# Optimization experiments

Measured on AMD Instinct MI355X. Metric: run time of the kernel, lower is better.

The kernel has to match this reference:

```python
import math
import jax, jax.numpy as jnp
import numpy as np

EPS = 1e-5  # BatchNorm2d default eps


def setup_inputs() -> dict:
    key = jax.random.key(0)
    ks = jax.random.split(key, 12)
    C, I = 256, 128  # in_channels, inter_channels (= C // reduction)
    n, h, w = 4, 64, 64
    s = 0.02
    return {
        "x": jax.random.normal(ks[0], (n, C, h, w), jnp.float32),
        "g_w": jax.random.normal(ks[1], (I, C), jnp.float32) * s,
        "g_b": jax.random.normal(ks[2], (I,), jnp.float32) * s,
        "theta_w": jax.random.normal(ks[3], (I, C), jnp.float32) * s,
        "theta_b": jax.random.normal(ks[4], (I,), jnp.float32) * s,
        "phi_w": jax.random.normal(ks[5], (I, C), jnp.float32) * s,
        "phi_b": jax.random.normal(ks[6], (I,), jnp.float32) * s,
        "out_w": jax.random.normal(ks[7], (C, I), jnp.float32) * s,
        "bn_gamma": jax.random.uniform(ks[8], (C,), jnp.float32, 0.5, 1.5),
        "bn_beta": jax.random.normal(ks[9], (C,), jnp.float32) * s,
        "bn_mean": jax.random.normal(ks[10], (C,), jnp.float32) * s,
        "bn_var": jax.random.uniform(ks[11], (C,), jnp.float32, 0.5, 1.5),
    }


def reference(x, g_w, g_b, theta_w, theta_b, phi_w, phi_b, out_w,
              bn_gamma, bn_beta, bn_mean, bn_var):
    n, c, h, w = x.shape
    xf = x.reshape(n, c, h * w)  # (n, C, N)

    def proj(Wm, b):  # 1x1 conv == per-position linear: (n, I, N)
        return jnp.einsum('ic,ncp->nip', Wm, xf) + b[None, :, None]

    g_x = proj(g_w, g_b)          # (n, I, N)
    theta_x = proj(theta_w, theta_b)  # (n, I, N)
    phi_x = proj(phi_w, phi_b)        # (n, I, N)

    # dot_product mode: softmax FIRST, then divide by sqrt(C) (faithful to source)
    scores = jnp.einsum('nip,niq->npq', theta_x, phi_x)  # (n, N, N)
    attn = jax.nn.softmax(scores, axis=-1) / math.sqrt(c)

    y = jnp.einsum('npq,niq->nip', attn, g_x)  # (n, I, N)
    y = y.reshape(n, -1, h, w)                 # (n, I, h, w)

    # conv_out: 1x1 conv (no bias) + BatchNorm2d (eval-mode running stats)
    y = jnp.einsum('oi,nihw->nohw', out_w, y)  # (n, C, h, w)
    inv = bn_gamma / jnp.sqrt(bn_var + EPS)
    y = y * inv[None, :, None, None] + (bn_beta - bn_mean * inv)[None, :, None, None]
    return y + x
```

## Files before the change

### kernel.cpp

```cpp
#include <hip/hip_runtime.h>

typedef short short8 __attribute__((ext_vector_type(8)));
typedef short short4v __attribute__((ext_vector_type(4)));
typedef float f32x4 __attribute__((ext_vector_type(4)));
typedef float f32x16 __attribute__((ext_vector_type(16)));
typedef unsigned int uint4v __attribute__((ext_vector_type(4)));
typedef unsigned int uint2v __attribute__((ext_vector_type(2)));

#define NB 4
#define CD 256
#define ID 128
#define NP 4096

static __device__ __forceinline__ short f2bf(float f){
  unsigned u = __float_as_uint(f);
  u += 0x7FFF + ((u >> 16) & 1);
  return (short)(u >> 16);
}
static __device__ __forceinline__ float bf2f(short s){
  unsigned u = ((unsigned)(unsigned short)s) << 16;
  return __uint_as_float(u);
}
static __device__ __forceinline__ unsigned cvtpk(float lo, float hi){
  unsigned r;
  asm("v_cvt_pk_bf16_f32 %0, %1, %2" : "=v"(r) : "v"(lo), "v"(hi));
  return r;
}
static __device__ __forceinline__ float fexp2(float x){
  float r;
  asm("v_exp_f32 %0, %1" : "=v"(r) : "v"(x));
  return r;
}
static __device__ __forceinline__ unsigned pack4_fp8(float a, float b, float c, float d){
  unsigned lo, hi;
  asm("v_cvt_pk_fp8_f32 %0, %1, %2" : "=v"(lo) : "v"(a), "v"(b));
  asm("v_cvt_pk_fp8_f32 %0, %1, %2" : "=v"(hi) : "v"(c), "v"(d));
  return (lo & 0xffffu) | (hi << 16);
}
static __device__ __forceinline__ unsigned char f2fp8(float v){
  unsigned u;
  asm("v_cvt_pk_fp8_f32 %0, %1, %1" : "=v"(u) : "v"(v));
  return (unsigned char)u;
}

static __device__ __forceinline__ void gload16(const void* g, void* l){
  __builtin_amdgcn_global_load_lds(
      (const __attribute__((address_space(1))) unsigned int*)g,
      (__attribute__((address_space(3))) unsigned int*)l, 16, 0, 0);
}

__global__ __launch_bounds__(256) void k_cvtw(const float* __restrict__ g_w,
    const float* __restrict__ th_w, const float* __restrict__ ph_w,
    const float* __restrict__ out_w, short* __restrict__ wb){
  int idx = (blockIdx.x * 256 + threadIdx.x) * 4;
  const float* s;
  int sel = idx >> 15;
  if(sel == 0) s = g_w; else if(sel == 1) s = th_w; else if(sel == 2) s = ph_w; else s = out_w;
  int off = idx & 32767;
  float4 v = *reinterpret_cast<const float4*>(s + off);
  short4v o = { f2bf(v.x), f2bf(v.y), f2bf(v.z), f2bf(v.w) };
  *reinterpret_cast<short4v*>(wb + idx) = o;
}

__global__ __launch_bounds__(256) void k_transpose(const float* __restrict__ x,
                                                   short* __restrict__ xt){
  __shared__ float T[64][68];
  int n = blockIdx.z, c0 = blockIdx.y * 64, p0 = blockIdx.x * 64;
  int t = threadIdx.x;
  const float* xp = x + ((size_t)(n * CD + c0)) * NP + p0;
#pragma unroll
  for(int it = 0; it < 4; ++it){
    int c = (t >> 4) + it * 16;
    int p = (t & 15) * 4;
    float4 v = *reinterpret_cast<const float4*>(xp + (size_t)c * NP + p);
    T[c][p+0] = v.x; T[c][p+1] = v.y; T[c][p+2] = v.z; T[c][p+3] = v.w;
  }
  __syncthreads();
  short* op = xt + ((size_t)(n * NP + p0)) * CD + c0;
  int p = t >> 2, cc = (t & 3) * 16;
  short8 a, b;
#pragma unroll
  for(int j = 0; j < 8; ++j){ a[j] = f2bf(T[cc + j][p]); b[j] = f2bf(T[cc + 8 + j][p]); }
  *reinterpret_cast<short8*>(op + (size_t)p * CD + cc) = a;
  *reinterpret_cast<short8*>(op + (size_t)p * CD + cc + 8) = b;
}

__global__ __launch_bounds__(512) void k_proj(const short* __restrict__ xt,
    const short* __restrict__ wb, const float* __restrict__ g_b,
    const float* __restrict__ th_b, const float* __restrict__ ph_b,
    unsigned char* __restrict__ q8, unsigned char* __restrict__ k8,
    unsigned char* __restrict__ v8){
  __shared__ __align__(16) char XT[32768];
  int b = blockIdx.x;
  int n = b >> 6, pt = b & 63;
  int pb0 = pt * 64;
  int t = threadIdx.x, w = t >> 6, l = t & 63;
  int lr = l & 15, lg = l >> 4;
  int i0 = w * 16;

  const char* xg = (const char*)(xt + ((size_t)(n * NP + pb0)) * CD);
#pragma unroll
  for(int i_ = 0; i_ < 4; ++i_){
    int dd = t * 16 + i_ * 8192;
    int row = dd >> 9;
    int sz = (dd & ~511) | ((dd & 511) ^ ((row & 15) << 4));
    gload16(xg + sz, XT + dd);
  }

  const short* gww = wb;
  const short* thw = wb + 32768;
  const short* phw = wb + 65536;
  short8 Wt[8], Wp[8], Wg[8];
#pragma unroll
  for(int kk = 0; kk < 8; ++kk){
    size_t wo = (size_t)(i0 + lr) * CD + kk * 32 + lg * 8;
    Wt[kk] = *reinterpret_cast<const short8*>(thw + wo);
    Wp[kk] = *reinterpret_cast<const short8*>(phw + wo);
    Wg[kk] = *reinterpret_cast<const short8*>(gww + wo);
  }
  float bt = th_b[i0 + lr] * 1.44269504f;
  float bp = ph_b[i0 + lr];
  float gb[4];
#pragma unroll
  for(int r = 0; r < 4; ++r) gb[r] = g_b[i0 + lg * 4 + r];

  __syncthreads();

  size_t pan = ((size_t)n * 64 + pt) * 64;
#pragma unroll
  for(int psub = 0; psub < 4; ++psub){
    int prow = psub * 16 + lr;
    short8 X[8];
#pragma unroll
    for(int kk = 0; kk < 8; ++kk)
      X[kk] = *reinterpret_cast<const short8*>(
          XT + prow * 512 + ((kk * 64 + lg * 16) ^ ((prow & 15) << 4)));
    f32x4 aT = {0.f,0.f,0.f,0.f}, aP = {0.f,0.f,0.f,0.f}, aG = {0.f,0.f,0.f,0.f};
#pragma unroll
    for(int kk = 0; kk < 8; ++kk){
      aT = __builtin_amdgcn_mfma_f32_16x16x32_bf16(X[kk], Wt[kk], aT, 0, 0, 0);
      aP = __builtin_amdgcn_mfma_f32_16x16x32_bf16(X[kk], Wp[kk], aP, 0, 0, 0);
      aG = __builtin_amdgcn_mfma_f32_16x16x32_bf16(Wg[kk], X[kk], aG, 0, 0, 0);
    }
#pragma unroll
    for(int r = 0; r < 4; ++r){
      size_t o = ((size_t)(n * NP + pb0 + psub * 16 + lg * 4 + r)) * ID + i0 + lr;
      q8[o] = f2fp8((aT[r] + bt * 0.69314718f * 1.44269504f));
    }
#pragma unroll
    for(int r = 0; r < 4; ++r){
      size_t o = ((size_t)(n * NP + pb0 + psub * 16 + lg * 4 + r)) * ID + i0 + lr;
      q8[o] = f2fp8((aT[r] + ph_b[0] * 0.f + th_b[i0 + lr]) * 1.44269504f);
      k8[o] = f2fp8(aP[r] + bp);
    }
#pragma unroll
    for(int r = 0; r < 4; ++r){
      int ii = i0 + lg * 4 + r;
      v8[(pan + (ii >> 1)) * 128 + (ii & 1) * 64 + psub * 16 + lr] = f2fp8(aG[r] + gb[r]);
    }
  }
}

__global__ __launch_bounds__(256, 2) void k_attn(const unsigned char* __restrict__ q8,
    const unsigned char* __restrict__ k8, const unsigned char* __restrict__ v8,
    short* __restrict__ po, float* __restrict__ psums){
  __shared__ __align__(16) char smem[65536];
  int b = blockIdx.x;
  int xcd = b & 7;
  int n = xcd >> 1;
  int kq = ((xcd & 1) << 1) | ((b >> 3) & 1);
  int qtl = b >> 4;
  int t = threadIdx.x, w = t >> 6, l = t & 63;
  int q31 = l & 31, hi = l >> 5;
  int pbase = qtl * 128 + w * 32;

  const char* kpanel = (const char*)k8 + ((size_t)(n * NP + kq * 1024)) * ID;
  const char* vpanel = (const char*)v8 + ((size_t)n * 64 + kq * 16) * 8192;
  const char* qbase  = (const char*)q8 + ((size_t)(n * NP + pbase)) * ID;

  uint2v Qf[8];
#pragma unroll
  for(int cst = 0; cst < 8; ++cst)
    Qf[cst] = *reinterpret_cast<const uint2v*>(qbase + q31 * 128 + cst * 16 + hi * 8);

  f32x16 Of[4];
#pragma unroll
  for(int db = 0; db < 4; ++db)
#pragma unroll
    for(int r = 0; r < 16; ++r) Of[db][r] = 0.f;
  float ps = 0.f;

#define STAGE(cb, kt_) do { \
    const char* kg_ = kpanel + (size_t)(kt_) * 8192; \
    const char* vg_ = vpanel + (size_t)(kt_) * 8192; \
    char* kld_ = smem + (cb) * 8192; \
    char* vld_ = smem + 16384 + (cb) * 8192; \
    _Pragma("unroll") \
    for(int i_ = 0; i_ < 2; ++i_){ \
      int dd = t * 16 + i_ * 4096; \
      int sz = (dd & ~127) | ((dd & 127) ^ (((dd >> 7) & 7) << 4)); \
      gload16(kg_ + sz, kld_ + dd); \
      gload16(vg_ + sz, vld_ + dd); \
    } \
  } while(0)

  STAGE(0, 0);
  __syncthreads();

#pragma unroll 2
  for(int kt = 0; kt < 16; ++kt){
    const int pb = kt & 1;
    if(kt + 1 < 16) STAGE(pb ^ 1, kt + 1);
    const char* Kc = smem + pb * 8192;
    const char* Vc = smem + 16384 + pb * 8192;
#pragma unroll
    for(int kb = 0; kb < 2; ++kb){
      f32x16 S;
#pragma unroll
      for(int r = 0; r < 16; ++r) S[r] = 0.f;
      int krow = kb * 32 + q31;
      __builtin_amdgcn_s_setprio(1);
#pragma unroll
      for(int cst = 0; cst < 8; ++cst){
        uint2v Kf = *reinterpret_cast<const uint2v*>(
            Kc + krow * 128 + ((cst * 16) ^ ((krow & 7) << 4)) + hi * 8);
        S = __builtin_amdgcn_mfma_f32_32x32x16_fp8_fp8(
            __builtin_bit_cast(long, Kf), __builtin_bit_cast(long, Qf[cst]), S, 0, 0, 0);
      }
      __builtin_amdgcn_s_setprio(0);
      float e[16];
#pragma unroll
      for(int r = 0; r < 16; ++r) e[r] = fexp2(S[r] - 4.0f);
#pragma unroll
      for(int r = 0; r < 16; ++r) ps += e[r];
      unsigned u0 = pack4_fp8(e[0],  e[1],  e[2],  e[3]);
      unsigned u1 = pack4_fp8(e[4],  e[5],  e[6],  e[7]);
      unsigned u2 = pack4_fp8(e[8],  e[9],  e[10], e[11]);
      unsigned u3 = pack4_fp8(e[12], e[13], e[14], e[15]);
      asm("v_permlane32_swap_b32 %0, %1" : "+v"(u0), "+v"(u1));
      asm("v_permlane32_swap_b32 %0, %1" : "+v"(u2), "+v"(u3));
      __builtin_amdgcn_s_setprio(1);
#pragma unroll
      for(int cc = 0; cc < 2; ++cc){
        uint2v Pa = cc ? uint2v{u2, u3} : uint2v{u0, u1};
        long Pl = __builtin_bit_cast(long, Pa);
#pragma unroll
        for(int db = 0; db < 4; ++db){
          int d = db * 32 + q31;
          int row = d >> 1;
          int off = (d & 1) * 64 + kb * 32 + cc * 16;
          uint2v Vf = *reinterpret_cast<const uint2v*>(
              Vc + row * 128 + ((off ^ ((row & 7) << 4))) + hi * 8);
          Of[db] = __builtin_amdgcn_mfma_f32_32x32x16_fp8_fp8(
              Pl, __builtin_bit_cast(long, Vf), Of[db], 0, 0, 0);
        }
      }
      __builtin_amdgcn_s_setprio(0);
    }
    __syncthreads();
  }
#undef STAGE

  float pst = ps + __shfl_xor(ps, 32);
  if(hi == 0)
    psums[(size_t)kq * 16384 + n * NP + pbase + q31] = pst;

  float* ow = (float*)(smem + w * 16384);
#pragma unroll
  for(int reg = 0; reg < 16; ++reg){
    int q = (reg & 3) + 8 * (reg >> 2) + 4 * hi;
#pragma unroll
    for(int db = 0; db < 4; ++db)
      ow[q * 128 + db * 32 + q31] = Of[db][reg];
  }
  asm volatile("s_waitcnt lgkmcnt(0)" ::: "memory");
  __builtin_amdgcn_sched_barrier(0);
  short* pr = po + ((size_t)kq * 16384 + n * NP + pbase) * ID;
#pragma unroll
  for(int it = 0; it < 8; ++it){
    int o = it * 1024 + l * 16;
    int q = o >> 8, d0 = (o & 255) >> 1;
    f32x4 va = *reinterpret_cast<const f32x4*>(ow + q * 128 + d0);
    f32x4 vb = *reinterpret_cast<const f32x4*>(ow + q * 128 + d0 + 4);
    uint4v pk4 = { cvtpk(va[0], va[1]), cvtpk(va[2], va[3]),
                   cvtpk(vb[0], vb[1]), cvtpk(vb[2], vb[3]) };
    *reinterpret_cast<short8*>(pr + (size_t)q * ID + d0) = __builtin_bit_cast(short8, pk4);
  }
}

__global__ __launch_bounds__(512) void k_outproj(const short* __restrict__ po,
    const float* __restrict__ psums, const short* __restrict__ ow_b,
    const float* __restrict__ bng, const float* __restrict__ bnb,
    const float* __restrict__ bnm, const float* __restrict__ bnv,
    const float* __restrict__ x, float* __restrict__ out){
  __shared__ __align__(16) short XW[64 * 128];
  int b = blockIdx.x;
  int n = b >> 6, pt = b & 63;
  int pg0 = pt * 64;
  int t = threadIdx.x, w = t >> 6, l = t & 63;
  int lr = l & 15, lg = l >> 4;

  {
    int p = t >> 3, i0 = (t & 7) * 16;
    size_t qg = (size_t)n * NP + pg0 + p;
    float den = psums[qg] + psums[16384 + qg] + psums[32768 + qg] + psums[49152 + qg];
    float inv = 1.f / (16.f * den);
    const short* pp = po + qg * ID + i0;
    int key = (p & 15) << 4;
#pragma unroll
    for(int h = 0; h < 2; ++h){
      short8 b0 = *reinterpret_cast<const short8*>(pp + h * 8);
      short8 b1 = *reinterpret_cast<const short8*>(pp + (size_t)16384 * ID + h * 8);
      short8 b2 = *reinterpret_cast<const short8*>(pp + (size_t)32768 * ID + h * 8);
      short8 b3 = *reinterpret_cast<const short8*>(pp + (size_t)49152 * ID + h * 8);
      float f[8];
#pragma unroll
      for(int j = 0; j < 8; ++j)
        f[j] = (bf2f(b0[j]) + bf2f(b1[j]) + bf2f(b2[j]) + bf2f(b3[j])) * inv;
      uint4v pkv = { cvtpk(f[0], f[1]), cvtpk(f[2], f[3]),
                     cvtpk(f[4], f[5]), cvtpk(f[6], f[7]) };
      *reinterpret_cast<short8*>((char*)XW + p * 256 + ((i0 * 2 + h * 16) ^ key)) =
          __builtin_bit_cast(short8, pkv);
    }
  }
  __syncthreads();

  int c0 = w * 32;
  f32x4 acc[2][4];
#pragma unroll
  for(int mf = 0; mf < 2; ++mf)
#pragma unroll
    for(int nf = 0; nf < 4; ++nf) acc[mf][nf] = {0.f,0.f,0.f,0.f};
#pragma unroll
  for(int kk = 0; kk < 4; ++kk){
    short8 Af[2];
#pragma unroll
    for(int mf = 0; mf < 2; ++mf)
      Af[mf] = *reinterpret_cast<const short8*>(ow_b + (size_t)(c0 + mf * 16 + lr) * ID + kk * 32 + lg * 8);
#pragma unroll
    for(int nf = 0; nf < 4; ++nf){
      int prow = nf * 16 + lr;
      short8 Bf = *reinterpret_cast<const short8*>(
          (char*)XW + prow * 256 + ((kk * 64 + lg * 16) ^ ((prow & 15) << 4)));
#pragma unroll
      for(int mf = 0; mf < 2; ++mf)
        acc[mf][nf] = __builtin_amdgcn_mfma_f32_16x16x32_bf16(Af[mf], Bf, acc[mf][nf], 0, 0, 0);
    }
  }

#pragma unroll
  for(int mf = 0; mf < 2; ++mf){
    int cb = c0 + mf * 16 + lg * 4;
    float inv[4], sh[4];
#pragma unroll
    for(int r = 0; r < 4; ++r){
      float iv = bng[cb + r] * rsqrtf(bnv[cb + r] + 1e-5f);
      inv[r] = iv;
      sh[r] = bnb[cb + r] - bnm[cb + r] * iv;
    }
#pragma unroll
    for(int nf = 0; nf < 4; ++nf){
      int p = pg0 + nf * 16 + lr;
#pragma unroll
      for(int r = 0; r < 4; ++r){
        size_t idx = ((size_t)(n * CD + cb + r)) * NP + p;
        out[idx] = acc[mf][nf][r] * inv[r] + sh[r] + x[idx];
      }
    }
  }
}

extern "C" void kernel_launch(void* const* d_in, const int* in_sizes, int n_in,
                              void* d_out, int out_size, void* d_ws, size_t ws_size,
                              hipStream_t stream){
  const float* x    = (const float*)d_in[0];
  const float* g_w  = (const float*)d_in[1];
  const float* g_b  = (const float*)d_in[2];
  const float* th_w = (const float*)d_in[3];
  const float* th_b = (const float*)d_in[4];
  const float* ph_w = (const float*)d_in[5];
  const float* ph_b = (const float*)d_in[6];
  const float* out_w= (const float*)d_in[7];
  const float* bng  = (const float*)d_in[8];
  const float* bnb  = (const float*)d_in[9];
  const float* bnm  = (const float*)d_in[10];
  const float* bnv  = (const float*)d_in[11];
  float* out = (float*)d_out;
  char* ws = (char*)d_ws;

  short* xt          = (short*)(ws);
  unsigned char* q8  = (unsigned char*)(ws + (size_t)(8u  << 20));
  unsigned char* k8  = (unsigned char*)(ws + (size_t)(12u << 20));
  unsigned char* v8  = (unsigned char*)(ws + (size_t)(16u << 20));
  short* wb          = (short*)(ws + (size_t)(24u << 20));
  short* po          = (short*)(ws + (size_t)(25u << 20));
  float* psum        = (float*)(ws + (size_t)(41u << 20));

  k_cvtw<<<128, 256, 0, stream>>>(g_w, th_w, ph_w, out_w, wb);
  k_transpose<<<dim3(64, 4, 4), 256, 0, stream>>>(x, xt);
  k_proj<<<256, 512, 0, stream>>>(xt, wb, g_b, th_b, ph_b, q8, k8, v8);
  k_attn<<<512, 256, 0, stream>>>(q8, k8, v8, po, psum);
  k_outproj<<<256, 512, 0, stream>>>(po, psum, wb + 98304, bng, bnb, bnm, bnv, x, out);
}
```

Before: 68.74 us.

## Process two query sub-tiles per wave in attention, halving block size

```diff
diff --git a/kernel.cpp b/kernel.cpp
--- a/kernel.cpp
+++ b/kernel.cpp
@@ -118,7 +118,7 @@
     Wp[kk] = *reinterpret_cast<const short8*>(phw + wo);
     Wg[kk] = *reinterpret_cast<const short8*>(gww + wo);
   }
-  float bt = th_b[i0 + lr] * 1.44269504f;
+  float bt = th_b[i0 + lr];
   float bp = ph_b[i0 + lr];
   float gb[4];
 #pragma unroll
@@ -145,12 +145,7 @@
 #pragma unroll
     for(int r = 0; r < 4; ++r){
       size_t o = ((size_t)(n * NP + pb0 + psub * 16 + lg * 4 + r)) * ID + i0 + lr;
-      q8[o] = f2fp8((aT[r] + bt * 0.69314718f * 1.44269504f));
-    }
-#pragma unroll
-    for(int r = 0; r < 4; ++r){
-      size_t o = ((size_t)(n * NP + pb0 + psub * 16 + lg * 4 + r)) * ID + i0 + lr;
-      q8[o] = f2fp8((aT[r] + ph_b[0] * 0.f + th_b[i0 + lr]) * 1.44269504f);
+      q8[o] = f2fp8((aT[r] + bt) * 1.44269504f);
       k8[o] = f2fp8(aP[r] + bp);
     }
 #pragma unroll
@@ -161,10 +156,10 @@
   }
 }
 
-__global__ __launch_bounds__(256, 2) void k_attn(const unsigned char* __restrict__ q8,
+__global__ __launch_bounds__(128, 2) void k_attn(const unsigned char* __restrict__ q8,
     const unsigned char* __restrict__ k8, const unsigned char* __restrict__ v8,
     short* __restrict__ po, float* __restrict__ psums){
-  __shared__ __align__(16) char smem[65536];
+  __shared__ __align__(16) char smem[32768];
   int b = blockIdx.x;
   int xcd = b & 7;
   int n = xcd >> 1;
@@ -172,23 +167,28 @@
   int qtl = b >> 4;
   int t = threadIdx.x, w = t >> 6, l = t & 63;
   int q31 = l & 31, hi = l >> 5;
-  int pbase = qtl * 128 + w * 32;
+  int pbase = qtl * 128 + w * 64;
 
   const char* kpanel = (const char*)k8 + ((size_t)(n * NP + kq * 1024)) * ID;
   const char* vpanel = (const char*)v8 + ((size_t)n * 64 + kq * 16) * 8192;
   const char* qbase  = (const char*)q8 + ((size_t)(n * NP + pbase)) * ID;
 
-  uint2v Qf[8];
-#pragma unroll
-  for(int cst = 0; cst < 8; ++cst)
-    Qf[cst] = *reinterpret_cast<const uint2v*>(qbase + q31 * 128 + cst * 16 + hi * 8);
-
-  f32x16 Of[4];
-#pragma unroll
-  for(int db = 0; db < 4; ++db)
-#pragma unroll
-    for(int r = 0; r < 16; ++r) Of[db][r] = 0.f;
-  float ps = 0.f;
+  uint2v Qf[2][8];
+#pragma unroll
+  for(int qs = 0; qs < 2; ++qs)
+#pragma unroll
+    for(int cst = 0; cst < 8; ++cst)
+      Qf[qs][cst] = *reinterpret_cast<const uint2v*>(
+          qbase + (qs * 32 + q31) * 128 + cst * 16 + hi * 8);
+
+  f32x16 Of[2][4];
+#pragma unroll
+  for(int qs = 0; qs < 2; ++qs)
+#pragma unroll
+    for(int db = 0; db < 4; ++db)
+#pragma unroll
+      for(int r = 0; r < 16; ++r) Of[qs][db][r] = 0.f;
+  float ps[2] = {0.f, 0.f};
 
 #define STAGE(cb, kt_) do { \
     const char* kg_ = kpanel + (size_t)(kt_) * 8192; \
@@ -196,8 +196,8 @@
     char* kld_ = smem + (cb) * 8192; \
     char* vld_ = smem + 16384 + (cb) * 8192; \
     _Pragma("unroll") \
-    for(int i_ = 0; i_ < 2; ++i_){ \
-      int dd = t * 16 + i_ * 4096; \
+    for(int i_ = 0; i_ < 4; ++i_){ \
+      int dd = t * 16 + i_ * 2048; \
       int sz = (dd & ~127) | ((dd & 127) ^ (((dd >> 7) & 7) << 4)); \
       gload16(kg_ + sz, kld_ + dd); \
       gload16(vg_ + sz, vld_ + dd); \
@@ -215,35 +215,44 @@
     const char* Vc = smem + 16384 + pb * 8192;
 #pragma unroll
     for(int kb = 0; kb < 2; ++kb){
-      f32x16 S;
-#pragma unroll
-      for(int r = 0; r < 16; ++r) S[r] = 0.f;
+      f32x16 S0, S1;
+#pragma unroll
+      for(int r = 0; r < 16; ++r){ S0[r] = 0.f; S1[r] = 0.f; }
       int krow = kb * 32 + q31;
       __builtin_amdgcn_s_setprio(1);
 #pragma unroll
       for(int cst = 0; cst < 8; ++cst){
         uint2v Kf = *reinterpret_cast<const uint2v*>(
             Kc + krow * 128 + ((cst * 16) ^ ((krow & 7) << 4)) + hi * 8);
-        S = __builtin_amdgcn_mfma_f32_32x32x16_fp8_fp8(
-            __builtin_bit_cast(long, Kf), __builtin_bit_cast(long, Qf[cst]), S, 0, 0, 0);
+        long Kl = __builtin_bit_cast(long, Kf);
+        S0 = __builtin_amdgcn_mfma_f32_32x32x16_fp8_fp8(
+            Kl, __builtin_bit_cast(long, Qf[0][cst]), S0, 0, 0, 0);
+        S1 = __builtin_amdgcn_mfma_f32_32x32x16_fp8_fp8(
+            Kl, __builtin_bit_cast(long, Qf[1][cst]), S1, 0, 0, 0);
       }
       __builtin_amdgcn_s_setprio(0);
-      float e[16];
-#pragma unroll
-      for(int r = 0; r < 16; ++r) e[r] = fexp2(S[r] - 4.0f);
-#pragma unroll
-      for(int r = 0; r < 16; ++r) ps += e[r];
-      unsigned u0 = pack4_fp8(e[0],  e[1],  e[2],  e[3]);
-      unsigned u1 = pack4_fp8(e[4],  e[5],  e[6],  e[7]);
-      unsigned u2 = pack4_fp8(e[8],  e[9],  e[10], e[11]);
-      unsigned u3 = pack4_fp8(e[12], e[13], e[14], e[15]);
-      asm("v_permlane32_swap_b32 %0, %1" : "+v"(u0), "+v"(u1));
-      asm("v_permlane32_swap_b32 %0, %1" : "+v"(u2), "+v"(u3));
+      uint2v Pf[2][2];
+#pragma unroll
+      for(int qs = 0; qs < 2; ++qs){
+        float e[16];
+#pragma unroll
+        for(int r = 0; r < 16; ++r) e[r] = fexp2((qs ? S1[r] : S0[r]) - 4.0f);
+#pragma unroll
+        for(int r = 0; r < 16; ++r) ps[qs] += e[r];
+        unsigned u0 = pack4_fp8(e[0],  e[1],  e[2],  e[3]);
+        unsigned u1 = pack4_fp8(e[4],  e[5],  e[6],  e[7]);
+        unsigned u2 = pack4_fp8(e[8],  e[9],  e[10], e[11]);
+        unsigned u3 = pack4_fp8(e[12], e[13], e[14], e[15]);
+        asm("v_permlane32_swap_b32 %0, %1" : "+v"(u0), "+v"(u1));
+        asm("v_permlane32_swap_b32 %0, %1" : "+v"(u2), "+v"(u3));
+        Pf[qs][0] = uint2v{u0, u1};
+        Pf[qs][1] = uint2v{u2, u3};
+      }
       __builtin_amdgcn_s_setprio(1);
 #pragma unroll
       for(int cc = 0; cc < 2; ++cc){
-        uint2v Pa = cc ? uint2v{u2, u3} : uint2v{u0, u1};
-        long Pl = __builtin_bit_cast(long, Pa);
+        long P0 = __builtin_bit_cast(long, Pf[0][cc]);
+        long P1 = __builtin_bit_cast(long, Pf[1][cc]);
 #pragma unroll
         for(int db = 0; db < 4; ++db){
           int d = db * 32 + q31;
@@ -251,8 +260,9 @@
           int off = (d & 1) * 64 + kb * 32 + cc * 16;
           uint2v Vf = *reinterpret_cast<const uint2v*>(
               Vc + row * 128 + ((off ^ ((row & 7) << 4))) + hi * 8);
-          Of[db] = __builtin_amdgcn_mfma_f32_32x32x16_fp8_fp8(
-              Pl, __builtin_bit_cast(long, Vf), Of[db], 0, 0, 0);
+          long Vl = __builtin_bit_cast(long, Vf);
+          Of[0][db] = __builtin_amdgcn_mfma_f32_32x32x16_fp8_fp8(P0, Vl, Of[0][db], 0, 0, 0);
+          Of[1][db] = __builtin_amdgcn_mfma_f32_32x32x16_fp8_fp8(P1, Vl, Of[1][db], 0, 0, 0);
         }
       }
       __builtin_amdgcn_s_setprio(0);
@@ -261,30 +271,37 @@
   }
 #undef STAGE
 
-  float pst = ps + __shfl_xor(ps, 32);
-  if(hi == 0)
-    psums[(size_t)kq * 16384 + n * NP + pbase + q31] = pst;
-
+#pragma unroll
+  for(int qs = 0; qs < 2; ++qs){
+    float pst = ps[qs] + __shfl_xor(ps[qs], 32);
+    if(hi == 0)
+      psums[(size_t)kq * 16384 + n * NP + pbase + qs * 32 + q31] = pst;
+  }
   float* ow = (float*)(smem + w * 16384);
-#pragma unroll
-  for(int reg = 0; reg < 16; ++reg){
-    int q = (reg & 3) + 8 * (reg >> 2) + 4 * hi;
-#pragma unroll
-    for(int db = 0; db < 4; ++db)
-      ow[q * 128 + db * 32 + q31] = Of[db][reg];
-  }
-  asm volatile("s_waitcnt lgkmcnt(0)" ::: "memory");
-  __builtin_amdgcn_sched_barrier(0);
-  short* pr = po + ((size_t)kq * 16384 + n * NP + pbase) * ID;
-#pragma unroll
-  for(int it = 0; it < 8; ++it){
-    int o = it * 1024 + l * 16;
-    int q = o >> 8, d0 = (o & 255) >> 1;
-    f32x4 va = *reinterpret_cast<const f32x4*>(ow + q * 128 + d0);
-    f32x4 vb = *reinterpret_cast<const f32x4*>(ow + q * 128 + d0 + 4);
-    uint4v pk4 = { cvtpk(va[0], va[1]), cvtpk(va[2], va[3]),
-                   cvtpk(vb[0], vb[1]), cvtpk(vb[2], vb[3]) };
-    *reinterpret_cast<short8*>(pr + (size_t)q * ID + d0) = __builtin_bit_cast(short8, pk4);
+  short* prb = po + ((size_t)kq * 16384 + n * NP + pbase) * ID;
+#pragma unroll
+  for(int qs = 0; qs < 2; ++qs){
+#pragma unroll
+    for(int reg = 0; reg < 16; ++reg){
+      int q = (reg & 3) + 8 * (reg >> 2) + 4 * hi;
+#pragma unroll
+      for(int db = 0; db < 4; ++db)
+        ow[q * 128 + db * 32 + q31] = Of[qs][db][reg];
+    }
+    asm volatile("s_waitcnt lgkmcnt(0)" ::: "memory");
+    __builtin_amdgcn_sched_barrier(0);
+    short* pr = prb + (size_t)(qs * 32) * ID;
+#pragma unroll
+    for(int it = 0; it < 8; ++it){
+      int o = it * 1024 + l * 16;
+      int q = o >> 8, d0 = (o & 255) >> 1;
+      f32x4 va = *reinterpret_cast<const f32x4*>(ow + q * 128 + d0);
+      f32x4 vb = *reinterpret_cast<const f32x4*>(ow + q * 128 + d0 + 4);
+      uint4v pk4 = { cvtpk(va[0], va[1]), cvtpk(va[2], va[3]),
+                     cvtpk(vb[0], vb[1]), cvtpk(vb[2], vb[3]) };
+      *reinterpret_cast<short8*>(pr + (size_t)q * ID + d0) = __builtin_bit_cast(short8, pk4);
+    }
+    asm volatile("s_waitcnt lgkmcnt(0)" ::: "memory");
   }
 }
 
@@ -399,6 +416,6 @@
   k_cvtw<<<128, 256, 0, stream>>>(g_w, th_w, ph_w, out_w, wb);
   k_transpose<<<dim3(64, 4, 4), 256, 0, stream>>>(x, xt);
   k_proj<<<256, 512, 0, stream>>>(xt, wb, g_b, th_b, ph_b, q8, k8, v8);
-  k_attn<<<512, 256, 0, stream>>>(q8, k8, v8, po, psum);
+  k_attn<<<512, 128, 0, stream>>>(q8, k8, v8, po, psum);
   k_outproj<<<256, 512, 0, stream>>>(po, psum, wb + 98304, bng, bnb, bnm, bnv, x, out);
 }
```

Result: slower. 108.5 us (+57.8%).
